# Kernel optimization log

Measured on AMD Instinct MI355X. Metric: run time of the kernel, lower is better.

## Reference

```python
import jax, jax.numpy as jnp
import numpy as np

N_NODES = 50000
N_EDGES = 800000
IN_DIM = 128
EMB_DIM = 128
NUM_LAYER = 3
NUM_GRAPHS = 512
BN_EPS = 1e-5


def setup_inputs() -> dict:
    key = jax.random.key(0)
    ks = jax.random.split(key, 10)
    x = jax.random.normal(ks[0], (N_NODES, IN_DIM), jnp.float32)
    edge_index = jax.random.randint(ks[1], (2, N_EDGES), 0, N_NODES)
    batch = jnp.sort(jax.random.randint(ks[2], (N_NODES,), 0, NUM_GRAPHS))
    W = jax.random.normal(ks[3], (NUM_LAYER, EMB_DIM, EMB_DIM), jnp.float32) / np.sqrt(EMB_DIM)
    b_hidden = 0.01 * jax.random.normal(ks[4], (NUM_LAYER - 1, EMB_DIM), jnp.float32)
    bn_gamma = 1.0 + 0.1 * jax.random.normal(ks[5], (NUM_LAYER, EMB_DIM), jnp.float32)
    bn_beta = 0.1 * jax.random.normal(ks[6], (NUM_LAYER, EMB_DIM), jnp.float32)
    bn_mean = 0.1 * jax.random.normal(ks[7], (NUM_LAYER, EMB_DIM), jnp.float32)
    bn_var = jnp.ones((NUM_LAYER, EMB_DIM), jnp.float32)
    We = jax.random.normal(ks[8], (2 * EMB_DIM, 1), jnp.float32) / np.sqrt(2 * EMB_DIM)
    be = jnp.zeros((1,), jnp.float32)
    Wn = jax.random.normal(ks[9], (EMB_DIM, 1), jnp.float32) / np.sqrt(EMB_DIM)
    bn_bias = jnp.zeros((1,), jnp.float32)
    return dict(x=x, edge_index=edge_index, batch=batch, num_graphs=NUM_GRAPHS,
                W=W, b_hidden=b_hidden, bn_gamma=bn_gamma, bn_beta=bn_beta,
                bn_mean=bn_mean, bn_var=bn_var, We=We, be=be, Wn=Wn, bn_bias=bn_bias)


def batch_norm(x, gamma, beta, mean, var):
    # eval-mode BatchNorm1d with running stats
    return (x - mean) * jax.lax.rsqrt(var + BN_EPS) * gamma + beta


def gcn_propagate(h, edge_index, num_nodes):
    # symmetric-normalized GCN aggregation with self loops (edge_weight = 1)
    loop = jnp.arange(num_nodes)
    row = jnp.concatenate([edge_index[0], loop])
    col = jnp.concatenate([edge_index[1], loop])
    deg = jax.ops.segment_sum(jnp.ones(row.shape[0], h.dtype), row, num_segments=num_nodes)
    dis = jnp.where(deg > 0, jax.lax.rsqrt(jnp.maximum(deg, 1.0)), 0.0)
    norm = dis[row] * dis[col]  # [E+N]
    return jax.ops.segment_sum(norm[:, None] * h[row], col, num_segments=num_nodes)


def reg_mask(mask, seg, size):
    # mask: [S,1]; seg: [S] int segment ids; size graphs
    key_num = jax.ops.segment_sum(mask, seg, num_segments=size) + 1e-8
    env_num = jax.ops.segment_sum(1.0 - mask, seg, num_segments=size) + 1e-8
    non_zero = jax.ops.segment_sum((mask > 0).astype(jnp.float32), seg, num_segments=size)
    all_mask = jax.ops.segment_sum(jnp.ones_like(mask), seg, num_segments=size)
    return key_num, env_num, non_zero / all_mask


def _forward(x, W, b_hidden, bn_gamma, bn_beta, bn_mean, bn_var, We, be, Wn, bn_bias,
             edge_index, batch, num_graphs):
    N = x.shape[0]
    # layer 1: GCNConv(gfn=True) => BN then plain linear (no bias, no propagation)
    h = batch_norm(x, bn_gamma[0], bn_beta[0], bn_mean[0], bn_var[0]) @ W[0]
    h = jax.nn.relu(h)  # num_layer > 1; dropout is identity in eval
    n_hidden = W.shape[0] - 1
    for i in range(n_hidden):
        hb = batch_norm(h, bn_gamma[i + 1], bn_beta[i + 1], bn_mean[i + 1], bn_var[i + 1])
        h = gcn_propagate(hb @ W[i + 1], edge_index, N) + b_hidden[i]
        if i != n_hidden - 1:
            h = jax.nn.relu(h)
    node_rep = h  # [N, emb]

    row, col = edge_index[0], edge_index[1]
    D = node_rep.shape[1]
    node_key = jax.nn.sigmoid(node_rep @ Wn + bn_bias)  # [N,1]
    # cat([rep[row], rep[col]]) @ We == rep[row] @ We[:D] + rep[col] @ We[D:]
    edge_key = jax.nn.sigmoid(node_rep[row] @ We[:D] + node_rep[col] @ We[D:] + be)  # [E,1]

    node_key_num, node_env_num, nz_node_ratio = reg_mask(node_key, batch, num_graphs)
    edge_key_num, edge_env_num, nz_edge_ratio = reg_mask(edge_key, batch[row], num_graphs)
    return (node_key, edge_key, node_key_num, node_env_num,
            edge_key_num, edge_env_num, nz_node_ratio, nz_edge_ratio)


def reference(x, edge_index, batch, num_graphs, W, b_hidden, bn_gamma, bn_beta,
              bn_mean, bn_var, We, be, Wn, bn_bias):
    return _forward(x, W, b_hidden, bn_gamma, bn_beta, bn_mean, bn_var,
                    We, be, Wn, bn_bias, edge_index, batch, num_graphs)
```

## Files before the change

kernel.cpp:

```cpp
#include <hip/hip_runtime.h>
#include <cstddef>
#include <cstring>

#define NN 50000
#define NNP 50048
#define NE 800000
#define D 128
#define NG 512
#define BN_EPS 1e-5f
#define RSZC 25000
#define RSZF 12500
#define NCHUNK 64
#define CSZ 12500
#define EDGE_BLOCKS 256
#define NB 196

typedef __bf16 bf16_t;
typedef __bf16 bf16x8 __attribute__((ext_vector_type(8)));
typedef float f32x4 __attribute__((ext_vector_type(4)));

#define OFF_ACCN 0
#define OFF_ACCE 2048
#define OFF_CTR  4096
#define ZERO_FLOATS 4160
#define OFF_DIS  4160
#define OFF_COLP 54208
#define OFF_BSUM 104448
#define OFF_COLPL 104704
#define OFF_BP   154752
#define OFF_WPT  155264
#define OFF_PR   179840
#define OFF_PC   1781376
#define OFF_SRCS OFF_PR
#define OFF_TB   979840
#define OFF_HBFA 3382912
#define OFF_HBFB 6585984

#define O_NKEY 0
#define O_EKEY 50000
#define O_NKN  850000
#define O_NEN  850512
#define O_EKN  851024
#define O_EEN  851536
#define O_NZN  852048
#define O_NZE  852560

__device__ __forceinline__ float sigmoidf(float x) {
    return 1.0f / (1.0f + expf(-x));
}

__device__ __forceinline__ unsigned short f2bf_bits(float f) {
    bf16_t h = (bf16_t)f;
    unsigned short u;
    __builtin_memcpy(&u, &h, 2);
    return u;
}

__device__ __forceinline__ float bf_lo(unsigned int u) {
    return __uint_as_float(u << 16);
}
__device__ __forceinline__ float bf_hi(unsigned int u) {
    return __uint_as_float(u & 0xFFFF0000u);
}

__global__ __launch_bounds__(256) void count_prep(const int* __restrict__ ei,
                                                  unsigned short* __restrict__ PR,
                                                  unsigned short* __restrict__ PC,
                                                  const float* __restrict__ W,
                                                  const float* __restrict__ gamma,
                                                  const float* __restrict__ beta,
                                                  const float* __restrict__ mean,
                                                  const float* __restrict__ var,
                                                  bf16_t* __restrict__ Wpt,
                                                  float* __restrict__ bp,
                                                  float* __restrict__ zbase) {
    const int tid = threadIdx.x;
    if (blockIdx.z == 2) {
        if (blockIdx.x == 0 && blockIdx.y < 3 && tid < D) {
            int l = blockIdx.y;
            int j = tid;
            float acc = 0.f;
            for (int k = 0; k < D; ++k) {
                float a = gamma[l * D + k] * rsqrtf(var[l * D + k] + BN_EPS);
                float c = beta[l * D + k] - mean[l * D + k] * a;
                float w = W[l * D * D + k * D + j];
                Wpt[l * D * D + j * D + k] = (bf16_t)(a * w);
                acc = fmaf(c, w, acc);
            }
            bp[l * D + j] = acc;
        } else if (blockIdx.x == 1 && blockIdx.y == 0) {
            for (int i = tid; i < ZERO_FLOATS; i += 256) zbase[i] = 0.f;
        }
        return;
    }
    extern __shared__ int hist[];
    const int r = blockIdx.x, p = blockIdx.y, dirz = blockIdx.z;
    for (int i = tid; i < RSZC; i += 256) hist[i] = 0;
    __syncthreads();
    const int base = r * RSZC;
    const int4* ids = (const int4*)(ei + dirz * NE + p * CSZ);
    for (int i = tid; i < CSZ / 4; i += 256) {
        int4 v = ids[i];
        int d0 = v.x - base, d1 = v.y - base, d2 = v.z - base, d3 = v.w - base;
        if ((unsigned)d0 < RSZC) atomicAdd(&hist[d0], 1);
        if ((unsigned)d1 < RSZC) atomicAdd(&hist[d1], 1);
        if ((unsigned)d2 < RSZC) atomicAdd(&hist[d2], 1);
        if ((unsigned)d3 < RSZC) atomicAdd(&hist[d3], 1);
    }
    __syncthreads();
    unsigned short* dst = (dirz == 0 ? PR : PC) + p * NNP + base;
    for (int i = tid; i < RSZC; i += 256) dst[i] = (unsigned short)hist[i];
}

__global__ void csr_mid(const unsigned short* __restrict__ PR,
                        unsigned short* __restrict__ PC,
                        float* __restrict__ dis,
                        int* __restrict__ colpL, int* __restrict__ bsum) {
    __shared__ int s[256];
    int t = threadIdx.x;
    int i = blockIdx.x * 256 + t;
    int run = 0;
    if (i < NN) {
        int dg = 0;
#pragma unroll 8
        for (int k = 0; k < NCHUNK; ++k) dg += PR[k * NNP + i];
        dis[i] = rsqrtf((float)(dg + 1));
        for (int k = 0; k < NCHUNK; ++k) {
            int v = PC[k * NNP + i];
            PC[k * NNP + i] = (unsigned short)run;
            run += v;
        }
    }
    s[t] = run;
    __syncthreads();
    for (int o = 1; o < 256; o <<= 1) {
        int add = (t >= o) ? s[t - o] : 0;
        __syncthreads();
        s[t] += add;
        __syncthreads();
    }
    if (i < NN) colpL[i] = s[t] - run;
    if (t == 255) bsum[blockIdx.x] = s[255];
}

__global__ __launch_bounds__(256) void fill_gemm01(
    const int* __restrict__ ei, const int* __restrict__ colpL,
    const int* __restrict__ bsum, int* __restrict__ colp,
    const unsigned short* __restrict__ CPS, const float* __restrict__ dis,
    unsigned int* __restrict__ srcs,
    const float* __restrict__ X, const bf16_t* __restrict__ Bt0,
    const bf16_t* __restrict__ Bt1, const float* __restrict__ bias0,
    const float* __restrict__ bias1, bf16_t* __restrict__ out) {
    extern __shared__ __align__(16) unsigned short smem[];
    const int bid = blockIdx.x;
    const int tid = threadIdx.x;

    if (bid < NB) {
        int* s = (int*)smem;
        s[tid] = (tid < bid) ? bsum[tid] : 0;
        __syncthreads();
        for (int o = 128; o; o >>= 1) {
            if (tid < o) s[tid] += s[tid + o];
            __syncthreads();
        }
        int boff = s[0];
        int i = bid * 256 + tid;
        if (i < NN) colp[i] = colpL[i] + boff;
        if (i == NN) colp[NN] = NE;
        return;
    }

    if (bid < NB + 256) {
        int* curs = (int*)smem;
        int* pb = curs + RSZF;
        const int fb = bid - NB;
        const int r = fb & 3, p = fb >> 2;
        const int base = r * RSZF;
        {
            int v = (tid < NB) ? bsum[tid] : 0;
            pb[tid] = v;
            __syncthreads();
            for (int o = 1; o < 256; o <<= 1) {
                int add = (tid >= o) ? pb[tid - o] : 0;
                __syncthreads();
                pb[tid] += add;
                __syncthreads();
            }
            int ex = pb[tid] - v;
            __syncthreads();
            pb[tid] = ex;
            __syncthreads();
        }
        for (int i = tid; i < RSZF; i += 256) {
            int g = base + i;
            curs[i] = colpL[g] + pb[g >> 8] + CPS[p * NNP + g];
        }
        __syncthreads();
        const int4* rows = (const int4*)(ei + p * CSZ);
        const int4* cols = (const int4*)(ei + NE + p * CSZ);
        for (int i = tid; i < CSZ / 4; i += 256) {
            int4 rv = rows[i];
            int4 cv = cols[i];
            int d;
            d = cv.x - base;
            if ((unsigned)d < RSZF)
                srcs[atomicAdd(&curs[d], 1)] =
                    (unsigned int)rv.x | ((unsigned int)f2bf_bits(dis[rv.x]) << 16);
            d = cv.y - base;
            if ((unsigned)d < RSZF)
                srcs[atomicAdd(&curs[d], 1)] =
                    (unsigned int)rv.y | ((unsigned int)f2bf_bits(dis[rv.y]) << 16);
            d = cv.z - base;
            if ((unsigned)d < RSZF)
                srcs[atomicAdd(&curs[d], 1)] =
                    (unsigned int)rv.z | ((unsigned int)f2bf_bits(dis[rv.z]) << 16);
            d = cv.w - base;
            if ((unsigned)d < RSZF)
                srcs[atomicAdd(&curs[d], 1)] =
                    (unsigned int)rv.w | ((unsigned int)f2bf_bits(dis[rv.w]) << 16);
        }
        return;
    }

    unsigned short* Bs = smem;
    unsigned short* As = smem + 16384;
    const int wv = tid >> 6;
    const int lane = tid & 63;
    const int l15 = lane & 15;
    const int l4 = lane >> 4;
    const int row0 = (bid - NB - 256) * 64;

    for (int q = tid; q < 2048; q += 256) {
        int r = q >> 4, u = q & 15;
        *(uint4*)&Bs[r * 128 + (u ^ (r & 7)) * 8] = *(const uint4*)(Bt0 + r * D + u * 8);
    }

    bf16x8 afrag[4];
    {
        int r = row0 + wv * 16 + l15;
        int rc = (r < NN) ? r : (NN - 1);
#pragma unroll
        for (int kk = 0; kk < 4; ++kk) {
            int off = rc * D + kk * 32 + l4 * 8;
            float4 f0 = *(const float4*)(X + off);
            float4 f1 = *(const float4*)(X + off + 4);
            bf16x8 a;
            a[0] = (bf16_t)f0.x; a[1] = (bf16_t)f0.y;
            a[2] = (bf16_t)f0.z; a[3] = (bf16_t)f0.w;
            a[4] = (bf16_t)f1.x; a[5] = (bf16_t)f1.y;
            a[6] = (bf16_t)f1.z; a[7] = (bf16_t)f1.w;
            afrag[kk] = a;
        }
    }
    __syncthreads();

    const int rsw = l15 & 7;
    f32x4 acc[8];
#pragma unroll
    for (int n = 0; n < 8; ++n) acc[n] = (f32x4){0.f, 0.f, 0.f, 0.f};
#pragma unroll
    for (int n = 0; n < 8; ++n) {
#pragma unroll
        for (int kk = 0; kk < 4; ++kk) {
            bf16x8 bfrag = *(const bf16x8*)&Bs[(n * 16 + l15) * 128 + ((kk * 4 + l4) ^ rsw) * 8];
            acc[n] = __builtin_amdgcn_mfma_f32_16x16x32_bf16(afrag[kk], bfrag, acc[n], 0, 0, 0);
        }
    }
#pragma unroll
    for (int n = 0; n < 8; ++n) {
        int col = n * 16 + l15;
        float bv = bias0[col];
#pragma unroll
        for (int r = 0; r < 4; ++r) {
            int rl = wv * 16 + l4 * 4 + r;
            float v = fmaxf(acc[n][r] + bv, 0.f);
            int cs = ((col >> 3) ^ (rl & 7));
            As[rl * 128 + cs * 8 + (col & 7)] = f2bf_bits(v);
        }
    }
    __syncthreads();

    for (int q = tid; q < 2048; q += 256) {
        int r = q >> 4, u = q & 15;
        *(uint4*)&Bs[r * 128 + (u ^ (r & 7)) * 8] = *(const uint4*)(Bt1 + r * D + u * 8);
    }
    const int rl = wv * 16 + l15;
    bf16x8 af2[4];
#pragma unroll
    for (int kk = 0; kk < 4; ++kk) {
        int cs = (kk * 4 + l4) ^ (rl & 7);
        af2[kk] = *(const bf16x8*)&As[rl * 128 + cs * 8];
    }
    __syncthreads();

#pragma unroll
    for (int n = 0; n < 8; ++n) acc[n] = (f32x4){0.f, 0.f, 0.f, 0.f};
#pragma unroll
    for (int n = 0; n < 8; ++n) {
#pragma unroll
        for (int kk = 0; kk < 4; ++kk) {
            bf16x8 bfrag = *(const bf16x8*)&Bs[(n * 16 + l15) * 128 + ((kk * 4 + l4) ^ rsw) * 8];
            acc[n] = __builtin_amdgcn_mfma_f32_16x16x32_bf16(af2[kk], bfrag, acc[n], 0, 0, 0);
        }
    }
#pragma unroll
    for (int n = 0; n < 8; ++n) {
        int col = n * 16 + l15;
        float bv = bias1[col];
#pragma unroll
        for (int r = 0; r < 4; ++r) {
            int row = row0 + wv * 16 + l4 * 4 + r;
            if (row < NN) out[(size_t)row * D + col] = (bf16_t)(acc[n][r] + bv);
        }
    }
}

__global__ __launch_bounds__(256) void gemm2(const bf16_t* __restrict__ A,
                                             const bf16_t* __restrict__ Bt,
                                             const float* __restrict__ bias,
                                             bf16_t* __restrict__ out) {
    __shared__ __align__(16) unsigned short Bs[128 * 128];
    const int tid = threadIdx.x;
    const int wv = tid >> 6;
    const int lane = tid & 63;
    const int l15 = lane & 15;
    const int l4 = lane >> 4;
    const int row0 = blockIdx.x * 64 + wv * 16;

    for (int q = tid; q < 2048; q += 256) {
        int r = q >> 4, u = q & 15;
        *(uint4*)&Bs[r * 128 + (u ^ (r & 7)) * 8] = *(const uint4*)(Bt + r * D + u * 8);
    }

    bf16x8 afrag[4];
    {
        int r = row0 + l15;
        int rc = (r < NN) ? r : (NN - 1);
#pragma unroll
        for (int kk = 0; kk < 4; ++kk)
            afrag[kk] = *(const bf16x8*)(A + rc * D + kk * 32 + l4 * 8);
    }
    __syncthreads();

    const int rsw = l15 & 7;
    f32x4 acc[8];
#pragma unroll
    for (int n = 0; n < 8; ++n) acc[n] = (f32x4){0.f, 0.f, 0.f, 0.f};
#pragma unroll
    for (int n = 0; n < 8; ++n) {
#pragma unroll
        for (int kk = 0; kk < 4; ++kk) {
            bf16x8 bfrag = *(const bf16x8*)&Bs[(n * 16 + l15) * 128 + ((kk * 4 + l4) ^ rsw) * 8];
            acc[n] = __builtin_amdgcn_mfma_f32_16x16x32_bf16(afrag[kk], bfrag, acc[n], 0, 0, 0);
        }
    }
#pragma unroll
    for (int n = 0; n < 8; ++n) {
        int col = n * 16 + l15;
        float bv = bias[col];
#pragma unroll
        for (int r = 0; r < 4; ++r) {
            int row = row0 + l4 * 4 + r;
            if (row < NN) out[(size_t)row * D + col] = (bf16_t)(acc[n][r] + bv);
        }
    }
}

template <int POST>
__global__ __launch_bounds__(256) void prop_gather(
    const int* __restrict__ colp,
    const unsigned int* __restrict__ srcs, const float* __restrict__ dis,
    const bf16_t* __restrict__ hin, bf16_t* __restrict__ hout,
    const float* __restrict__ bias) {
    int n = blockIdx.x * 4 + (threadIdx.x >> 6);
    n = __builtin_amdgcn_readfirstlane(n);
    int lane = threadIdx.x & 63;
    if (n >= NN) return;
    const int start = colp[n];
    const int end = colp[n + 1];
    const float dn = dis[n];
    unsigned int u = ((const unsigned int*)(hin + (size_t)n * D))[lane];
    float ax = dn * bf_lo(u), ay = dn * bf_hi(u);
    int i = start;
    for (; i + 3 < end; i += 4) {
        unsigned int e0 = srcs[i], e1 = srcs[i + 1], e2 = srcs[i + 2], e3 = srcs[i + 3];
        unsigned int u0 = ((const unsigned int*)(hin + (size_t)(e0 & 0xFFFFu) * D))[lane];
        unsigned int u1 = ((const unsigned int*)(hin + (size_t)(e1 & 0xFFFFu) * D))[lane];
        unsigned int u2 = ((const unsigned int*)(hin + (size_t)(e2 & 0xFFFFu) * D))[lane];
        unsigned int u3 = ((const unsigned int*)(hin + (size_t)(e3 & 0xFFFFu) * D))[lane];
        float w0 = bf_hi(e0), w1 = bf_hi(e1), w2 = bf_hi(e2), w3 = bf_hi(e3);
        ax = fmaf(w0, bf_lo(u0), ax); ay = fmaf(w0, bf_hi(u0), ay);
        ax = fmaf(w1, bf_lo(u1), ax); ay = fmaf(w1, bf_hi(u1), ay);
        ax = fmaf(w2, bf_lo(u2), ax); ay = fmaf(w2, bf_hi(u2), ay);
        ax = fmaf(w3, bf_lo(u3), ax); ay = fmaf(w3, bf_hi(u3), ay);
    }
    for (; i < end; ++i) {
        unsigned int e0 = srcs[i];
        unsigned int u0 = ((const unsigned int*)(hin + (size_t)(e0 & 0xFFFFu) * D))[lane];
        float w0 = bf_hi(e0);
        ax = fmaf(w0, bf_lo(u0), ax); ay = fmaf(w0, bf_hi(u0), ay);
    }
    float vx = dn * ax, vy = dn * ay;
    if (POST == 0) {
        float2 bb = ((const float2*)bias)[lane];
        vx = fmaxf(vx + bb.x, 0.f);
        vy = fmaxf(vy + bb.y, 0.f);
    }
    unsigned int pk = (unsigned int)f2bf_bits(vx) | ((unsigned int)f2bf_bits(vy) << 16);
    ((unsigned int*)(hout + (size_t)n * D))[lane] = pk;
}

__global__ __launch_bounds__(256) void node_kernel(
    const bf16_t* __restrict__ h, const float* __restrict__ bh1,
    const float* __restrict__ We, const float* __restrict__ Wn,
    const float* __restrict__ bnb, const int* __restrict__ batch,
    float* __restrict__ nkey_out, float4* __restrict__ tb,
    float* __restrict__ accN) {
    __shared__ float binK[NG], binE[NG], binZ[NG], binC[NG];
    const int tid = threadIdx.x;
    for (int i = tid; i < NG; i += 256) { binK[i] = 0.f; binE[i] = 0.f; binZ[i] = 0.f; binC[i] = 0.f; }
    __syncthreads();

    const int CHUNK = 98;
    int start = blockIdx.x * CHUNK;
    int end = min(start + CHUNK, NN);
    int sub = tid >> 5;
    int l32 = tid & 31;
    float bnb0 = bnb[0];

    float4 w1 = ((const float4*)We)[l32];
    float4 w2 = ((const float4*)(We + D))[l32];
    float4 wn = ((const float4*)Wn)[l32];
    float4 bb = ((const float4*)bh1)[l32];

    for (int n = start + sub; n < end; n += 8) {
        uint2 pk = ((const uint2*)(h + (size_t)n * D))[l32];
        float v0 = bf_lo(pk.x) + bb.x;
        float v1 = bf_hi(pk.x) + bb.y;
        float v2 = bf_lo(pk.y) + bb.z;
        float v3 = bf_hi(pk.y) + bb.w;
        float s1 = v0 * w1.x + v1 * w1.y + v2 * w1.z + v3 * w1.w;
        float s2 = v0 * w2.x + v1 * w2.y + v2 * w2.z + v3 * w2.w;
        float s3 = v0 * wn.x + v1 * wn.y + v2 * wn.z + v3 * wn.w;
        for (int o = 16; o; o >>= 1) {
            s1 += __shfl_xor(s1, o);
            s2 += __shfl_xor(s2, o);
            s3 += __shfl_xor(s3, o);
        }
        if (l32 == 0) {
            float nk = sigmoidf(s3 + bnb0);
            nkey_out[n] = nk;
            int g = batch[n];
            tb[n] = make_float4(s1, s2, __int_as_float(g), 0.f);
            atomicAdd(&binK[g], nk);
            atomicAdd(&binE[g], 1.0f - nk);
            if (nk > 0.f) atomicAdd(&binZ[g], 1.0f);
            atomicAdd(&binC[g], 1.0f);
        }
    }
    __syncthreads();
    if (start < NN) {
        int glo = batch[start];
        int ghi = batch[end - 1];
        for (int g = glo + tid; g <= ghi; g += 256) {
            unsafeAtomicAdd(&accN[g], binK[g]);
            unsafeAtomicAdd(&accN[NG + g], binE[g]);
            unsafeAtomicAdd(&accN[2 * NG + g], binZ[g]);
            unsafeAtomicAdd(&accN[3 * NG + g], binC[g]);
        }
    }
}

__global__ __launch_bounds__(256) void edge_final(
    const int* __restrict__ ei, const float4* __restrict__ tb,
    const float* __restrict__ be, float* __restrict__ ekey_out,
    float* __restrict__ accE, const float* __restrict__ accN,
    int* __restrict__ ctr, float* __restrict__ out) {
    __shared__ float binK[NG], binE[NG], binZ[NG], binC[NG];
    __shared__ int isLast;
    const int tid = threadIdx.x;
    for (int i = tid; i < NG; i += 256) { binK[i] = 0.f; binE[i] = 0.f; binZ[i] = 0.f; binC[i] = 0.f; }
    __syncthreads();
    float be0 = be[0];
    int stride4 = gridDim.x * 256;
    for (int q = blockIdx.x * 256 + tid; q < NE / 4; q += stride4) {
        int4 r4 = ((const int4*)ei)[q];
        int4 c4 = ((const int4*)(ei + NE))[q];
        float4 tr0 = tb[r4.x], tr1 = tb[r4.y], tr2 = tb[r4.z], tr3 = tb[r4.w];
        float4 tc0 = tb[c4.x], tc1 = tb[c4.y], tc2 = tb[c4.z], tc3 = tb[c4.w];
        int g0 = __float_as_int(tr0.z), g1 = __float_as_int(tr1.z);
        int g2 = __float_as_int(tr2.z), g3 = __float_as_int(tr3.z);
        float e0 = sigmoidf(tr0.x + tc0.y + be0);
        float e1 = sigmoidf(tr1.x + tc1.y + be0);
        float e2 = sigmoidf(tr2.x + tc2.y + be0);
        float e3 = sigmoidf(tr3.x + tc3.y + be0);
        ((float4*)ekey_out)[q] = make_float4(e0, e1, e2, e3);
        atomicAdd(&binK[g0], e0); atomicAdd(&binE[g0], 1.0f - e0);
        if (e0 > 0.f) atomicAdd(&binZ[g0], 1.0f);
        atomicAdd(&binC[g0], 1.0f);
        atomicAdd(&binK[g1], e1); atomicAdd(&binE[g1], 1.0f - e1);
        if (e1 > 0.f) atomicAdd(&binZ[g1], 1.0f);
        atomicAdd(&binC[g1], 1.0f);
        atomicAdd(&binK[g2], e2); atomicAdd(&binE[g2], 1.0f - e2);
        if (e2 > 0.f) atomicAdd(&binZ[g2], 1.0f);
        atomicAdd(&binC[g2], 1.0f);
        atomicAdd(&binK[g3], e3); atomicAdd(&binE[g3], 1.0f - e3);
        if (e3 > 0.f) atomicAdd(&binZ[g3], 1.0f);
        atomicAdd(&binC[g3], 1.0f);
    }
    __syncthreads();
    for (int g = tid; g < NG; g += 256) {
        if (binC[g] != 0.f) {
            unsafeAtomicAdd(&accE[g], binK[g]);
            unsafeAtomicAdd(&accE[NG + g], binE[g]);
            unsafeAtomicAdd(&accE[2 * NG + g], binZ[g]);
            unsafeAtomicAdd(&accE[3 * NG + g], binC[g]);
        }
    }
    __syncthreads();
    if (tid == 0) {
        __threadfence();
        int old = atomicAdd(ctr, 1);
        isLast = (old == (int)gridDim.x - 1);
    }
    __syncthreads();
    if (isLast) {
        __threadfence();
        for (int g = tid; g < NG; g += 256) {
            out[O_NKN + g] = accN[g] + 1e-8f;
            out[O_NEN + g] = accN[NG + g] + 1e-8f;
            out[O_EKN + g] = accE[g] + 1e-8f;
            out[O_EEN + g] = accE[NG + g] + 1e-8f;
            out[O_NZN + g] = accN[2 * NG + g] / accN[3 * NG + g];
            out[O_NZE + g] = accE[2 * NG + g] / accE[3 * NG + g];
        }
    }
}

extern "C" void kernel_launch(void* const* d_in, const int* in_sizes, int n_in,
                              void* d_out, int out_size, void* d_ws, size_t ws_size,
                              hipStream_t stream) {
    const float* x     = (const float*)d_in[0];
    const int*   ei    = (const int*)d_in[1];
    const int*   batch = (const int*)d_in[2];
    const float* W     = (const float*)d_in[4];
    const float* bh    = (const float*)d_in[5];
    const float* gamma = (const float*)d_in[6];
    const float* beta  = (const float*)d_in[7];
    const float* mean  = (const float*)d_in[8];
    const float* var   = (const float*)d_in[9];
    const float* We    = (const float*)d_in[10];
    const float* be    = (const float*)d_in[11];
    const float* Wn    = (const float*)d_in[12];
    const float* bnb   = (const float*)d_in[13];

    float* ws  = (float*)d_ws;
    float* out = (float*)d_out;

    float*          accN  = ws + OFF_ACCN;
    float*          accE  = ws + OFF_ACCE;
    int*            ctr   = (int*)(ws + OFF_CTR);
    float*          dis   = ws + OFF_DIS;
    int*            colp  = (int*)(ws + OFF_COLP);
    int*            bsum  = (int*)(ws + OFF_BSUM);
    int*            colpL = (int*)(ws + OFF_COLPL);
    float*          bp    = ws + OFF_BP;
    bf16_t*         Wpt   = (bf16_t*)(ws + OFF_WPT);
    unsigned short* PR    = (unsigned short*)(ws + OFF_PR);
    unsigned short* PC    = (unsigned short*)(ws + OFF_PC);
    unsigned int*   srcs  = (unsigned int*)(ws + OFF_SRCS);
    float4*         tb    = (float4*)(ws + OFF_TB);
    bf16_t*         hbfA  = (bf16_t*)(ws + OFF_HBFA);
    bf16_t*         hbfB  = (bf16_t*)(ws + OFF_HBFB);

    count_prep<<<dim3(2, NCHUNK, 3), 256, RSZC * sizeof(int), stream>>>(
        ei, PR, PC, W, gamma, beta, mean, var, Wpt, bp, ws);
    csr_mid<<<NB, 256, 0, stream>>>(PR, PC, dis, colpL, bsum);

    const int GB = (NN + 63) / 64;
    fill_gemm01<<<NB + 256 + GB, 256, 51024, stream>>>(
        ei, colpL, bsum, colp, PC, dis, srcs,
        x, Wpt, Wpt + D * D, bp, bp + D, hbfB);
    prop_gather<0><<<12500, 256, 0, stream>>>(colp, srcs, dis, hbfB, hbfA, bh);
    gemm2<<<GB, 256, 0, stream>>>(hbfA, Wpt + 2 * D * D, bp + 2 * D, hbfB);
    prop_gather<1><<<12500, 256, 0, stream>>>(colp, srcs, dis, hbfB, hbfA, nullptr);

    node_kernel<<<512, 256, 0, stream>>>(hbfA, bh + D, We, Wn, bnb, batch,
                                         out + O_NKEY, tb, accN);
    edge_final<<<EDGE_BLOCKS, 256, 0, stream>>>(ei, tb, be, out + O_EKEY,
                                                accE, accN, ctr, out);
}
```

Baseline: 196.1 us.

## Fuse csr_mid with layer-0/1 GEMM and split CSR fill into separate kernel

Moves the degree/prefix computation of csr_mid into the blocks of the combined GEMM kernel, so the independent GEMM work for layers 0-1 runs alongside the CSR mid-pass. The colp scan and edge fill move into a new scan_fill kernel launched afterwards. The kernel count stays the same, but the CSR pipeline is regrouped so the dense GEMM overlaps the mid-scan instead of the fill. The GEMM kernel now requests slightly less shared memory, which may affect occupancy.

New measurement: 208.1 us. 6.1% more time.

```diff
diff --git a/kernel.cpp b/kernel.cpp
--- a/kernel.cpp
+++ b/kernel.cpp
@@ -93,61 +93,28 @@
         }
         return;
     }
-    extern __shared__ int hist[];
+    extern __shared__ int histi[];
     const int r = blockIdx.x, p = blockIdx.y, dirz = blockIdx.z;
-    for (int i = tid; i < RSZC; i += 256) hist[i] = 0;
+    for (int i = tid; i < RSZC; i += 256) histi[i] = 0;
     __syncthreads();
     const int base = r * RSZC;
     const int4* ids = (const int4*)(ei + dirz * NE + p * CSZ);
     for (int i = tid; i < CSZ / 4; i += 256) {
         int4 v = ids[i];
         int d0 = v.x - base, d1 = v.y - base, d2 = v.z - base, d3 = v.w - base;
-        if ((unsigned)d0 < RSZC) atomicAdd(&hist[d0], 1);
-        if ((unsigned)d1 < RSZC) atomicAdd(&hist[d1], 1);
-        if ((unsigned)d2 < RSZC) atomicAdd(&hist[d2], 1);
-        if ((unsigned)d3 < RSZC) atomicAdd(&hist[d3], 1);
+        if ((unsigned)d0 < RSZC) atomicAdd(&histi[d0], 1);
+        if ((unsigned)d1 < RSZC) atomicAdd(&histi[d1], 1);
+        if ((unsigned)d2 < RSZC) atomicAdd(&histi[d2], 1);
+        if ((unsigned)d3 < RSZC) atomicAdd(&histi[d3], 1);
     }
     __syncthreads();
     unsigned short* dst = (dirz == 0 ? PR : PC) + p * NNP + base;
-    for (int i = tid; i < RSZC; i += 256) dst[i] = (unsigned short)hist[i];
-}
-
-__global__ void csr_mid(const unsigned short* __restrict__ PR,
-                        unsigned short* __restrict__ PC,
-                        float* __restrict__ dis,
-                        int* __restrict__ colpL, int* __restrict__ bsum) {
-    __shared__ int s[256];
-    int t = threadIdx.x;
-    int i = blockIdx.x * 256 + t;
-    int run = 0;
-    if (i < NN) {
-        int dg = 0;
-#pragma unroll 8
-        for (int k = 0; k < NCHUNK; ++k) dg += PR[k * NNP + i];
-        dis[i] = rsqrtf((float)(dg + 1));
-        for (int k = 0; k < NCHUNK; ++k) {
-            int v = PC[k * NNP + i];
-            PC[k * NNP + i] = (unsigned short)run;
-            run += v;
-        }
-    }
-    s[t] = run;
-    __syncthreads();
-    for (int o = 1; o < 256; o <<= 1) {
-        int add = (t >= o) ? s[t - o] : 0;
-        __syncthreads();
-        s[t] += add;
-        __syncthreads();
-    }
-    if (i < NN) colpL[i] = s[t] - run;
-    if (t == 255) bsum[blockIdx.x] = s[255];
-}
-
-__global__ __launch_bounds__(256) void fill_gemm01(
-    const int* __restrict__ ei, const int* __restrict__ colpL,
-    const int* __restrict__ bsum, int* __restrict__ colp,
-    const unsigned short* __restrict__ CPS, const float* __restrict__ dis,
-    unsigned int* __restrict__ srcs,
+    for (int i = tid; i < RSZC; i += 256) dst[i] = (unsigned short)histi[i];
+}
+
+__global__ __launch_bounds__(256) void csrmid_gemm01(
+    const unsigned short* __restrict__ PR, unsigned short* __restrict__ PC,
+    float* __restrict__ dis, int* __restrict__ colpL, int* __restrict__ bsum,
     const float* __restrict__ X, const bf16_t* __restrict__ Bt0,
     const bf16_t* __restrict__ Bt1, const float* __restrict__ bias0,
     const float* __restrict__ bias1, bf16_t* __restrict__ out) {
@@ -157,68 +124,29 @@
 
     if (bid < NB) {
         int* s = (int*)smem;
-        s[tid] = (tid < bid) ? bsum[tid] : 0;
+        int i = bid * 256 + tid;
+        int run = 0;
+        if (i < NN) {
+            int dg = 0;
+#pragma unroll 8
+            for (int k = 0; k < NCHUNK; ++k) dg += PR[k * NNP + i];
+            dis[i] = rsqrtf((float)(dg + 1));
+            for (int k = 0; k < NCHUNK; ++k) {
+                int v = PC[k * NNP + i];
+                PC[k * NNP + i] = (unsigned short)run;
+                run += v;
+            }
+        }
+        s[tid] = run;
         __syncthreads();
-        for (int o = 128; o; o >>= 1) {
-            if (tid < o) s[tid] += s[tid + o];
+        for (int o = 1; o < 256; o <<= 1) {
+            int add = (tid >= o) ? s[tid - o] : 0;
             __syncthreads();
-        }
-        int boff = s[0];
-        int i = bid * 256 + tid;
-        if (i < NN) colp[i] = colpL[i] + boff;
-        if (i == NN) colp[NN] = NE;
-        return;
-    }
-
-    if (bid < NB + 256) {
-        int* curs = (int*)smem;
-        int* pb = curs + RSZF;
-        const int fb = bid - NB;
-        const int r = fb & 3, p = fb >> 2;
-        const int base = r * RSZF;
-        {
-            int v = (tid < NB) ? bsum[tid] : 0;
-            pb[tid] = v;
+            s[tid] += add;
             __syncthreads();
-            for (int o = 1; o < 256; o <<= 1) {
-                int add = (tid >= o) ? pb[tid - o] : 0;
-                __syncthreads();
-                pb[tid] += add;
-                __syncthreads();
-            }
-            int ex = pb[tid] - v;
-            __syncthreads();
-            pb[tid] = ex;
-            __syncthreads();
-        }
-        for (int i = tid; i < RSZF; i += 256) {
-            int g = base + i;
-            curs[i] = colpL[g] + pb[g >> 8] + CPS[p * NNP + g];
-        }
-        __syncthreads();
-        const int4* rows = (const int4*)(ei + p * CSZ);
-        const int4* cols = (const int4*)(ei + NE + p * CSZ);
-        for (int i = tid; i < CSZ / 4; i += 256) {
-            int4 rv = rows[i];
-            int4 cv = cols[i];
-            int d;
-            d = cv.x - base;
-            if ((unsigned)d < RSZF)
-                srcs[atomicAdd(&curs[d], 1)] =
-                    (unsigned int)rv.x | ((unsigned int)f2bf_bits(dis[rv.x]) << 16);
-            d = cv.y - base;
-            if ((unsigned)d < RSZF)
-                srcs[atomicAdd(&curs[d], 1)] =
-                    (unsigned int)rv.y | ((unsigned int)f2bf_bits(dis[rv.y]) << 16);
-            d = cv.z - base;
-            if ((unsigned)d < RSZF)
-                srcs[atomicAdd(&curs[d], 1)] =
-                    (unsigned int)rv.z | ((unsigned int)f2bf_bits(dis[rv.z]) << 16);
-            d = cv.w - base;
-            if ((unsigned)d < RSZF)
-                srcs[atomicAdd(&curs[d], 1)] =
-                    (unsigned int)rv.w | ((unsigned int)f2bf_bits(dis[rv.w]) << 16);
-        }
+        }
+        if (i < NN) colpL[i] = s[tid] - run;
+        if (tid == 255) bsum[bid] = s[255];
         return;
     }
 
@@ -228,7 +156,7 @@
     const int lane = tid & 63;
     const int l15 = lane & 15;
     const int l4 = lane >> 4;
-    const int row0 = (bid - NB - 256) * 64;
+    const int row0 = (bid - NB) * 64;
 
     for (int q = tid; q < 2048; q += 256) {
         int r = q >> 4, u = q & 15;
@@ -312,6 +240,80 @@
             int row = row0 + wv * 16 + l4 * 4 + r;
             if (row < NN) out[(size_t)row * D + col] = (bf16_t)(acc[n][r] + bv);
         }
+    }
+}
+
+__global__ __launch_bounds__(256) void scan_fill(
+    const int* __restrict__ ei, const int* __restrict__ colpL,
+    const int* __restrict__ bsum, int* __restrict__ colp,
+    const unsigned short* __restrict__ CPS, const float* __restrict__ dis,
+    unsigned int* __restrict__ srcs) {
+    extern __shared__ __align__(16) unsigned short smem[];
+    const int bid = blockIdx.x;
+    const int tid = threadIdx.x;
+
+    if (bid < NB) {
+        int* s = (int*)smem;
+        s[tid] = (tid < bid) ? bsum[tid] : 0;
+        __syncthreads();
+        for (int o = 128; o; o >>= 1) {
+            if (tid < o) s[tid] += s[tid + o];
+            __syncthreads();
+        }
+        int boff = s[0];
+        int i = bid * 256 + tid;
+        if (i < NN) colp[i] = colpL[i] + boff;
+        if (i == NN) colp[NN] = NE;
+        return;
+    }
+
+    int* curs = (int*)smem;
+    int* pb = curs + RSZF;
+    const int fb = bid - NB;
+    const int r = fb & 3, p = fb >> 2;
+    const int base = r * RSZF;
+    {
+        int v = (tid < NB) ? bsum[tid] : 0;
+        pb[tid] = v;
+        __syncthreads();
+        for (int o = 1; o < 256; o <<= 1) {
+            int add = (tid >= o) ? pb[tid - o] : 0;
+            __syncthreads();
+            pb[tid] += add;
+            __syncthreads();
+        }
+        int ex = pb[tid] - v;
+        __syncthreads();
+        pb[tid] = ex;
+        __syncthreads();
+    }
+    for (int i = tid; i < RSZF; i += 256) {
+        int g = base + i;
+        curs[i] = colpL[g] + pb[g >> 8] + CPS[p * NNP + g];
+    }
+    __syncthreads();
+    const int4* rows = (const int4*)(ei + p * CSZ);
+    const int4* cols = (const int4*)(ei + NE + p * CSZ);
+    for (int i = tid; i < CSZ / 4; i += 256) {
+        int4 rv = rows[i];
+        int4 cv = cols[i];
+        int d;
+        d = cv.x - base;
+        if ((unsigned)d < RSZF)
+            srcs[atomicAdd(&curs[d], 1)] =
+                (unsigned int)rv.x | ((unsigned int)f2bf_bits(dis[rv.x]) << 16);
+        d = cv.y - base;
+        if ((unsigned)d < RSZF)
+            srcs[atomicAdd(&curs[d], 1)] =
+                (unsigned int)rv.y | ((unsigned int)f2bf_bits(dis[rv.y]) << 16);
+        d = cv.z - base;
+        if ((unsigned)d < RSZF)
+            srcs[atomicAdd(&curs[d], 1)] =
+                (unsigned int)rv.z | ((unsigned int)f2bf_bits(dis[rv.z]) << 16);
+        d = cv.w - base;
+        if ((unsigned)d < RSZF)
+            srcs[atomicAdd(&curs[d], 1)] =
+                (unsigned int)rv.w | ((unsigned int)f2bf_bits(dis[rv.w]) << 16);
     }
 }
 
@@ -575,12 +577,12 @@
 
     count_prep<<<dim3(2, NCHUNK, 3), 256, RSZC * sizeof(int), stream>>>(
         ei, PR, PC, W, gamma, beta, mean, var, Wpt, bp, ws);
-    csr_mid<<<NB, 256, 0, stream>>>(PR, PC, dis, colpL, bsum);
 
     const int GB = (NN + 63) / 64;
-    fill_gemm01<<<NB + 256 + GB, 256, 51024, stream>>>(
-        ei, colpL, bsum, colp, PC, dis, srcs,
-        x, Wpt, Wpt + D * D, bp, bp + D, hbfB);
+    csrmid_gemm01<<<NB + GB, 256, 49152, stream>>>(
+        PR, PC, dis, colpL, bsum, x, Wpt, Wpt + D * D, bp, bp + D, hbfB);
+    scan_fill<<<NB + 256, 256, 51024, stream>>>(ei, colpL, bsum, colp, PC, dis, srcs);
+
     prop_gather<0><<<12500, 256, 0, stream>>>(colp, srcs, dis, hbfB, hbfA, bh);
     gemm2<<<GB, 256, 0, stream>>>(hbfA, Wpt + 2 * D * D, bp + 2 * D, hbfB);
     prop_gather<1><<<12500, 256, 0, stream>>>(colp, srcs, dis, hbfB, hbfA, nullptr);
```
